# Performance work log

Measured on AMD Instinct MI355X. Metric: run time of the kernel, lower is better.

Reference implementation:

```python
import jax, jax.numpy as jnp
import numpy as np

RADIUS = 16.0
N_SLOT = 112
N_HEAD = 8
DIM = 512
EPS = 1e-5  # LayerNorm eps (torch default)


def _l2norm(x, axis):
    # F.normalize: x / max(||x||, 1e-12)
    n = jnp.linalg.norm(x, axis=axis, keepdims=True)
    return x / jnp.maximum(n, 1e-12)


def _layernorm(x, g, b):
    m = jnp.mean(x, axis=-1, keepdims=True)
    v = jnp.var(x, axis=-1, keepdims=True)
    return (x - m) * jax.lax.rsqrt(v + EPS) * g + b


def setup_inputs() -> dict:
    key = jax.random.key(0)
    ks = jax.random.split(key, 8)
    B, S = 64, 512
    head_dim = 512 // N_HEAD
    return {
        "query": jax.random.normal(ks[0], (B, S, DIM), jnp.float32),
        "value": jax.random.normal(ks[1], (B, S, 512), jnp.float32),
        # learned memory (init normal(0, 0.5) as in the module)
        "mem_key": jax.random.normal(ks[2], (N_HEAD * N_SLOT, head_dim), jnp.float32) * 0.5,
        "mem_value": jax.random.normal(ks[3], (N_SLOT, 512), jnp.float32) * 0.5,
        # linear projections (weight stored torch-style as [out, in])
        "q_w": jax.random.normal(ks[4], (512, DIM), jnp.float32) * 0.02,
        "q_b": jnp.zeros((512,), jnp.float32),
        "v_w": jax.random.normal(ks[5], (512, 512), jnp.float32) * 0.02,
        "v_b": jnp.zeros((512,), jnp.float32),
        "out_w": jax.random.normal(ks[6], (512, 512 * N_HEAD), jnp.float32) * 0.02,
        "out_b": jnp.zeros((512,), jnp.float32),
        "ln1_g": jnp.ones((512,), jnp.float32),
        "ln1_b": jnp.zeros((512,), jnp.float32),
        "ln3_g": jnp.ones((512,), jnp.float32),
        "ln3_b": jnp.zeros((512,), jnp.float32),
    }


def reference(query, value, mem_key, mem_value, q_w, q_b, v_w, v_b,
              out_w, out_b, ln1_g, ln1_b, ln3_g, ln3_b):
    B, S, C = query.shape
    N = B * S
    # --- predict branch: multi-head cosine-sim addressing + softmax read ---
    key_n = _l2norm(mem_key.reshape(N_HEAD, N_SLOT, -1), axis=2)          # [h,s,d]
    qp = (query.reshape(N, C) @ q_w.T + q_b).reshape(N, N_HEAD, -1)       # [n,h,d]
    qp = _l2norm(qp, axis=2)
    key_sim = jnp.einsum('bhd,hsd->bhs', qp, key_n)                       # [n,h,slot]
    key_addr = jax.nn.softmax(RADIUS * key_sim, axis=2)
    m_head = jnp.einsum('bhs,sd->bhd', key_addr,
                        jax.lax.stop_gradient(mem_value))                 # value.detach()
    m_head = m_head.reshape(N, N_HEAD * 512)
    attn_out = m_head @ out_w.T + out_b                                   # [n,512]
    # dropout treated as identity (eval mode)
    f_predict = _layernorm(query + attn_out.reshape(B, S, -1), ln1_g, ln1_b)
    # --- recon branch (inference=False) ---
    v_flat = jax.lax.stop_gradient(value.reshape(N, -1))                  # value.detach()
    v_proj = v_flat @ v_w.T + v_b
    value_norm = _l2norm(mem_value, axis=1)                               # [slot,512]
    value_sim = _l2norm(v_proj, axis=1) @ value_norm.T                    # [n,slot]
    value_addr = jax.nn.softmax(RADIUS * value_sim, axis=1)
    attn_recon = value_addr @ mem_value                                   # [n,512]
    contrastive_loss = jnp.abs(jnp.eye(N_SLOT, dtype=mem_value.dtype)
                               - value_norm @ value_norm.T).sum() * 0.01
    cos = jnp.sum(_l2norm(attn_recon, 1) * _l2norm(v_flat, 1), axis=1)
    recon_loss = jnp.abs(1.0 - cos).sum() / N
    attn_recon = _layernorm(attn_recon, ln3_g, ln3_b)
    f_target_recon = _layernorm(query + attn_recon.reshape(B, S, -1), ln1_g, ln1_b)
    return (f_predict, f_target_recon, recon_loss, contrastive_loss)
```

## Files before the change

### kernel.cpp

```cpp
#include <hip/hip_runtime.h>
#include <hip/hip_bf16.h>
#include <math.h>

typedef __bf16 bf16_t;
typedef __attribute__((ext_vector_type(8))) __bf16 bf16x8;
typedef __attribute__((ext_vector_type(4))) __bf16 bf16x4;
typedef __attribute__((ext_vector_type(4))) float f32x4;

#define LN_EPS 1e-5f
#define RADIUS_F 16.0f

__device__ inline bf16x8 zero8() {
    bf16x8 v;
#pragma unroll
    for (int i = 0; i < 8; ++i) v[i] = (__bf16)0.f;
    return v;
}

__device__ inline float wave_sum(float v) {
#pragma unroll
    for (int o = 1; o < 64; o <<= 1) v += __shfl_xor(v, o);
    return v;
}

__device__ inline void gload_lds16(const bf16_t* g, bf16_t* l) {
    __builtin_amdgcn_global_load_lds(
        (const __attribute__((address_space(1))) void*)g,
        (__attribute__((address_space(3))) void*)l, 16, 0, 0);
}

__device__ inline void drain_barrier() {
    asm volatile("s_waitcnt vmcnt(0)" ::: "memory");
    __builtin_amdgcn_s_barrier();
}

__global__ __launch_bounds__(256) void cast_all(
    const float* __restrict__ q, const float* __restrict__ v,
    const float* __restrict__ qw, const float* __restrict__ vw,
    const float* __restrict__ ow,
    bf16_t* __restrict__ qb, bf16_t* __restrict__ vb,
    bf16_t* __restrict__ qwb, bf16_t* __restrict__ vwb,
    bf16_t* __restrict__ owb) {
    const int total = 9043968;
    for (int i = blockIdx.x * 256 + threadIdx.x; i < total; i += gridDim.x * 256) {
        const float* src;
        bf16_t* dst;
        int j;
        if (i < 4194304) { src = q; dst = qb; j = i; }
        else if (i < 8388608) { src = v; dst = vb; j = i - 4194304; }
        else if (i < 8454144) { src = qw; dst = qwb; j = i - 8388608; }
        else if (i < 8519680) { src = vw; dst = vwb; j = i - 8454144; }
        else { src = ow; dst = owb; j = i - 8519680; }
        float4 x = reinterpret_cast<const float4*>(src)[j];
        bf16x4 o;
        o[0] = (__bf16)x.x; o[1] = (__bf16)x.y; o[2] = (__bf16)x.z; o[3] = (__bf16)x.w;
        reinterpret_cast<bf16x4*>(dst)[j] = o;
    }
}

__global__ __launch_bounds__(256) void keyn_k(const float* __restrict__ mk,
                                              bf16_t* __restrict__ kn) {
    int row = blockIdx.x * 4 + (threadIdx.x >> 6);
    int lane = threadIdx.x & 63;
    float x = mk[(size_t)row * 64 + lane];
    float ss = wave_sum(x * x);
    kn[(size_t)row * 64 + lane] = (__bf16)(x / fmaxf(sqrtf(ss), 1e-12f));
}

__global__ __launch_bounds__(256) void mv_prep_k(const float* __restrict__ mv,
                                                 bf16_t* __restrict__ mvb,
                                                 bf16_t* __restrict__ mvT,
                                                 float* __restrict__ invmv,
                                                 float* __restrict__ loss_slots) {
    const int s = blockIdx.x, tid = threadIdx.x;
    if (s >= 112) {
        mvb[(size_t)s * 512 + tid * 2] = (__bf16)0.f;
        mvb[(size_t)s * 512 + tid * 2 + 1] = (__bf16)0.f;
        mvT[(size_t)tid * 128 + s] = (__bf16)0.f;
        mvT[(size_t)(tid + 256) * 128 + s] = (__bf16)0.f;
        return;
    }
    float2 x = *reinterpret_cast<const float2*>(mv + (size_t)s * 512 + tid * 2);
    float ss = wave_sum(x.x * x.x + x.y * x.y);
    __shared__ float red[4];
    int wid = tid >> 6, lane = tid & 63;
    if (lane == 0) red[wid] = ss;
    __syncthreads();
    ss = red[0] + red[1] + red[2] + red[3];
    if (tid == 0) invmv[s] = 1.f / fmaxf(sqrtf(ss), 1e-12f);
    mvb[(size_t)s * 512 + tid * 2] = (__bf16)x.x;
    mvb[(size_t)s * 512 + tid * 2 + 1] = (__bf16)x.y;
    mvT[(size_t)tid * 128 + s] = (__bf16)mv[(size_t)s * 512 + tid];
    mvT[(size_t)(tid + 256) * 128 + s] = (__bf16)mv[(size_t)s * 512 + tid + 256];
    if (s == 0 && tid < 2) loss_slots[tid] = 0.f;
}

__global__ __launch_bounds__(256) void contrastive_k(const float* __restrict__ mv,
                                                     const float* __restrict__ invmv,
                                                     float* __restrict__ out_slot) {
    const int a = blockIdx.x;
    const int tid = threadIdx.x, wid = tid >> 6, lane = tid & 63;
    __shared__ float rowa[512];
    __shared__ float wsum[4];
    for (int i = tid; i < 512; i += 256) rowa[i] = mv[(size_t)a * 512 + i];
    __syncthreads();
    float acc = 0.f;
    const float ia = invmv[a];
    for (int b = wid; b < 112; b += 4) {
        float d = 0.f;
#pragma unroll
        for (int i = 0; i < 8; ++i) d += rowa[lane + i * 64] * mv[(size_t)b * 512 + lane + i * 64];
        d = wave_sum(d);
        float gv = d * ia * invmv[b];
        acc += fabsf((a == b ? 1.f : 0.f) - gv);
    }
    if (lane == 0) wsum[wid] = acc;
    __syncthreads();
    if (tid == 0) atomicAdd(out_slot, (wsum[0] + wsum[1] + wsum[2] + wsum[3]) * 0.01f);
}

__global__ __launch_bounds__(256) void gemm128_bb(
    const bf16_t* __restrict__ A, int lda,
    const bf16_t* __restrict__ W, int ldw,
    const float* __restrict__ bias,
    bf16_t* __restrict__ Cb, int ldc, int K) {
    __shared__ __align__(16) bf16_t As[2][128 * 32];
    __shared__ __align__(16) bf16_t Bs[2][128 * 32];
    const int tid = threadIdx.x;
    const int wid = tid >> 6, lane = tid & 63;
    const int wr = wid >> 1, wc = wid & 1;
    const int lr = lane & 15;
    const int ko = (lane >> 4) * 8;
    const size_t rowBase = (size_t)blockIdx.x * 128;
    const size_t colBase = (size_t)blockIdx.y * 128;
    const int r0 = tid >> 2;
    const int c0 = (tid & 3) * 8;
    const bf16_t* a_src = A + (rowBase + r0) * lda + c0;
    const bf16_t* w_src = W + (colBase + r0) * ldw + c0;
    f32x4 acc[4][4];
#pragma unroll
    for (int m = 0; m < 4; ++m)
#pragma unroll
        for (int n = 0; n < 4; ++n) {
            acc[m][n][0] = 0.f; acc[m][n][1] = 0.f;
            acc[m][n][2] = 0.f; acc[m][n][3] = 0.f;
        }
    auto stage = [&](int buf, int ks) {
        const int k0 = ks * 32;
        gload_lds16(a_src + k0, &As[buf][tid * 8]);
        gload_lds16(a_src + (size_t)64 * lda + k0, &As[buf][2048 + tid * 8]);
        gload_lds16(w_src + k0, &Bs[buf][tid * 8]);
        gload_lds16(w_src + (size_t)64 * ldw + k0, &Bs[buf][2048 + tid * 8]);
    };
    stage(0, 0);
    __syncthreads();
    const int nt = K >> 5;
    int cur = 0;
    for (int ks = 0; ks < nt; ++ks) {
        const int nb = cur ^ 1;
        if (ks + 1 < nt) stage(nb, ks + 1);
        bf16x8 af[4], bfr[4];
#pragma unroll
        for (int m = 0; m < 4; ++m)
            af[m] = *reinterpret_cast<const bf16x8*>(&As[cur][(wr * 64 + m * 16 + lr) * 32 + ko]);
#pragma unroll
        for (int n = 0; n < 4; ++n)
            bfr[n] = *reinterpret_cast<const bf16x8*>(&Bs[cur][(wc * 64 + n * 16 + lr) * 32 + ko]);
#pragma unroll
        for (int m = 0; m < 4; ++m)
#pragma unroll
            for (int n = 0; n < 4; ++n)
                acc[m][n] = __builtin_amdgcn_mfma_f32_16x16x32_bf16(af[m], bfr[n], acc[m][n], 0, 0, 0);
        __syncthreads();
        cur = nb;
    }
    const int rj = (lane >> 4) * 4;
#pragma unroll
    for (int n = 0; n < 4; ++n) {
        const int col = (int)colBase + wc * 64 + n * 16 + lr;
        const float bv = bias ? bias[col] : 0.f;
#pragma unroll
        for (int m = 0; m < 4; ++m) {
            const size_t r = rowBase + wr * 64 + m * 16 + rj;
#pragma unroll
            for (int j = 0; j < 4; ++j)
                Cb[(r + j) * ldc + col] = (__bf16)(acc[m][n][j] + bv);
        }
    }
}

__global__ __launch_bounds__(256) void gemm_bt(
    const bf16_t* __restrict__ A, int lda, int aZ,
    const bf16_t* __restrict__ W, int ldw, int wZ,
    bf16_t* __restrict__ Cb, int ldc, int cZ,
    int M, int N, int K) {
    const int wid = threadIdx.x >> 6;
    const int lane = threadIdx.x & 63;
    const int lr = lane & 15;
    const int kk = (lane >> 4) * 8;
    const int row0 = blockIdx.x * 64 + wid * 16;
    const int col0 = blockIdx.y * 64;
    A += (size_t)blockIdx.z * aZ;
    W += (size_t)blockIdx.z * wZ;
    const bf16_t* a_ptr = A + (size_t)(row0 + lr) * lda + kk;
    const bf16_t* w_ptr = W + (size_t)(col0 + lr) * ldw + kk;
    f32x4 acc[4];
#pragma unroll
    for (int t = 0; t < 4; ++t) { acc[t][0] = 0.f; acc[t][1] = 0.f; acc[t][2] = 0.f; acc[t][3] = 0.f; }
    bool colv[4];
#pragma unroll
    for (int t = 0; t < 4; ++t) colv[t] = (col0 + t * 16 + lr) < N;
    for (int k0 = 0; k0 < K; k0 += 32) {
        bf16x8 a = *reinterpret_cast<const bf16x8*>(a_ptr + k0);
#pragma unroll
        for (int t = 0; t < 4; ++t) {
            bf16x8 b;
            if (colv[t]) b = *reinterpret_cast<const bf16x8*>(w_ptr + (size_t)t * 16 * ldw + k0);
            else b = zero8();
            acc[t] = __builtin_amdgcn_mfma_f32_16x16x32_bf16(a, b, acc[t], 0, 0, 0);
        }
    }
    const int rb = (lane >> 4) * 4;
    Cb += (size_t)blockIdx.z * cZ;
#pragma unroll
    for (int t = 0; t < 4; ++t) {
        int col = col0 + t * 16 + lr;
        if (col >= N) continue;
#pragma unroll
        for (int j = 0; j < 4; ++j) {
            int r = row0 + rb + j;
            Cb[(size_t)r * ldc + col] = (__bf16)acc[t][j];
        }
    }
}

__global__ __launch_bounds__(256) void addr_predict(const bf16_t* __restrict__ qp,
                                                    const bf16_t* __restrict__ keyn,
                                                    bf16_t* __restrict__ addr) {
    const int wid = threadIdx.x >> 6, lane = threadIdx.x & 63;
    const int lr = lane & 15, kk = (lane >> 4) * 8;
    const int h = blockIdx.y;
    const int row0 = blockIdx.x * 64 + wid * 16;
    const bf16_t* a_ptr = qp + (size_t)(row0 + lr) * 512 + h * 64 + kk;
    bf16x8 a0 = *reinterpret_cast<const bf16x8*>(a_ptr);
    bf16x8 a1 = *reinterpret_cast<const bf16x8*>(a_ptr + 32);
    float ssq = 0.f;
#pragma unroll
    for (int j = 0; j < 8; ++j) {
        float x = (float)a0[j], y = (float)a1[j];
        ssq += x * x + y * y;
    }
    ssq += __shfl_xor(ssq, 16);
    ssq += __shfl_xor(ssq, 32);
    const float invq = 1.f / fmaxf(sqrtf(ssq), 1e-12f);
    f32x4 acc[7];
#pragma unroll
    for (int t = 0; t < 7; ++t) {
        const bf16_t* b_ptr = keyn + (size_t)(h * 112 + t * 16 + lr) * 64 + kk;
        bf16x8 b0 = *reinterpret_cast<const bf16x8*>(b_ptr);
        bf16x8 b1 = *reinterpret_cast<const bf16x8*>(b_ptr + 32);
        f32x4 c; c[0] = 0.f; c[1] = 0.f; c[2] = 0.f; c[3] = 0.f;
        c = __builtin_amdgcn_mfma_f32_16x16x32_bf16(a0, b0, c, 0, 0, 0);
        c = __builtin_amdgcn_mfma_f32_16x16x32_bf16(a1, b1, c, 0, 0, 0);
        acc[t] = c;
    }
    const int rb = (lane >> 4) * 4;
    float iq[4];
#pragma unroll
    for (int j = 0; j < 4; ++j) iq[j] = __shfl(invq, rb + j);
#pragma unroll
    for (int j = 0; j < 4; ++j) {
        float m = -1e30f;
#pragma unroll
        for (int t = 0; t < 7; ++t) { acc[t][j] *= iq[j] * RADIUS_F; m = fmaxf(m, acc[t][j]); }
#pragma unroll
        for (int o = 1; o < 16; o <<= 1) m = fmaxf(m, __shfl_xor(m, o));
        float s = 0.f;
#pragma unroll
        for (int t = 0; t < 7; ++t) { float e = __expf(acc[t][j] - m); acc[t][j] = e; s += e; }
#pragma unroll
        for (int o = 1; o < 16; o <<= 1) s += __shfl_xor(s, o);
        const float rs = 1.f / s;
#pragma unroll
        for (int t = 0; t < 7; ++t) acc[t][j] *= rs;
    }
#pragma unroll
    for (int t = 0; t < 7; ++t)
#pragma unroll
        for (int j = 0; j < 4; ++j)
            addr[(size_t)(row0 + rb + j) * 896 + h * 112 + t * 16 + lr] = (__bf16)acc[t][j];
}

__global__ __launch_bounds__(256, 2) void gemm_sim_softmax(
    const bf16_t* __restrict__ vp,
    const bf16_t* __restrict__ mvb,
    const float* __restrict__ invmv,
    bf16_t* __restrict__ addr2) {
    __shared__ __align__(16) bf16_t As[2][128 * 32];
    __shared__ __align__(16) bf16_t Bs[2][128 * 32];
    const int tid = threadIdx.x;
    const int wid = tid >> 6, lane = tid & 63;
    const int lr = lane & 15, hi = lane >> 4;
    const int ko = hi * 8;
    const size_t rowBase = (size_t)blockIdx.x * 128;
    const int r0 = tid >> 2, c0 = (tid & 3) * 8;
    const bf16_t* a_src = vp + (rowBase + r0) * 512 + c0;
    const bf16_t* b_src = mvb + (size_t)r0 * 512 + c0;
    f32x4 acc[2][8];
#pragma unroll
    for (int m = 0; m < 2; ++m)
#pragma unroll
        for (int n = 0; n < 8; ++n) {
            acc[m][n][0] = 0.f; acc[m][n][1] = 0.f;
            acc[m][n][2] = 0.f; acc[m][n][3] = 0.f;
        }
    float ssq[2] = {0.f, 0.f};
    auto stage = [&](int buf, int ks) {
        const int k0 = ks * 32;
        gload_lds16(a_src + k0, &As[buf][tid * 8]);
        gload_lds16(a_src + (size_t)64 * 512 + k0, &As[buf][2048 + tid * 8]);
        gload_lds16(b_src + k0, &Bs[buf][tid * 8]);
        gload_lds16(b_src + (size_t)64 * 512 + k0, &Bs[buf][2048 + tid * 8]);
    };
    stage(0, 0);
    drain_barrier();
    int cur = 0;
    for (int ks = 0; ks < 16; ++ks) {
        if (ks < 15) stage(cur ^ 1, ks + 1);
        bf16x8 af[2], bfr[8];
#pragma unroll
        for (int m = 0; m < 2; ++m)
            af[m] = *reinterpret_cast<const bf16x8*>(&As[cur][(wid * 32 + m * 16 + lr) * 32 + ko]);
#pragma unroll
        for (int n = 0; n < 8; ++n)
            bfr[n] = *reinterpret_cast<const bf16x8*>(&Bs[cur][(n * 16 + lr) * 32 + ko]);
#pragma unroll
        for (int m = 0; m < 2; ++m) {
#pragma unroll
            for (int j = 0; j < 8; ++j) { float x = (float)af[m][j]; ssq[m] += x * x; }
#pragma unroll
            for (int n = 0; n < 8; ++n)
                acc[m][n] = __builtin_amdgcn_mfma_f32_16x16x32_bf16(af[m], bfr[n], acc[m][n], 0, 0, 0);
        }
        drain_barrier();
        cur ^= 1;
    }
#pragma unroll
    for (int m = 0; m < 2; ++m) {
        ssq[m] += __shfl_xor(ssq[m], 16);
        ssq[m] += __shfl_xor(ssq[m], 32);
        ssq[m] = 1.f / fmaxf(sqrtf(ssq[m]), 1e-12f);
    }
    const int rb = hi * 4;
    float imv[7];
#pragma unroll
    for (int n = 0; n < 7; ++n) imv[n] = invmv[n * 16 + lr];
#pragma unroll
    for (int m = 0; m < 2; ++m)
#pragma unroll
        for (int j = 0; j < 4; ++j) {
            const float iq = __shfl(ssq[m], (lane & 48) | (rb + j));
            float x[7];
            float mx = -1e30f;
#pragma unroll
            for (int n = 0; n < 7; ++n) {
                x[n] = acc[m][n][j] * iq * imv[n] * RADIUS_F;
                mx = fmaxf(mx, x[n]);
            }
#pragma unroll
            for (int o = 1; o < 16; o <<= 1) mx = fmaxf(mx, __shfl_xor(mx, o));
            float s = 0.f;
#pragma unroll
            for (int n = 0; n < 7; ++n) { x[n] = __expf(x[n] - mx); s += x[n]; }
#pragma unroll
            for (int o = 1; o < 16; o <<= 1) s += __shfl_xor(s, o);
            const float rs = 1.f / s;
            const size_t row = rowBase + wid * 32 + m * 16 + rb + j;
#pragma unroll
            for (int n = 0; n < 7; ++n)
                addr2[row * 128 + n * 16 + lr] = (__bf16)(x[n] * rs);
            addr2[row * 128 + 112 + lr] = (__bf16)0.f;
        }
}

__global__ __launch_bounds__(256) void fused_ep(
    const bf16_t* __restrict__ sP, const bf16_t* __restrict__ sR,
    const bf16_t* __restrict__ qb, const bf16_t* __restrict__ vb,
    const float* __restrict__ g1, const float* __restrict__ b1,
    const float* __restrict__ g3, const float* __restrict__ b3,
    float* __restrict__ fP, float* __restrict__ fR,
    float* __restrict__ rrpart) {
    const int wid = threadIdx.x >> 6, lane = threadIdx.x & 63;
    const size_t row0 = (size_t)blockIdx.x * 8 + wid * 2;
    const int c1 = lane * 8, c2 = lane * 8 + 4;
    float xP[2][8], aR[2][8], qv[2][8];
    float s1[2], s2[2], sa[2], sa2[2], sav[2], sv2[2];
#pragma unroll
    for (int r = 0; r < 2; ++r) {
        const size_t base = (row0 + r) * 512;
        bf16x8 p = *reinterpret_cast<const bf16x8*>(sP + base + c1);
        bf16x8 rr = *reinterpret_cast<const bf16x8*>(sR + base + c1);
        bf16x8 qq = *reinterpret_cast<const bf16x8*>(qb + base + c1);
        bf16x8 vv = *reinterpret_cast<const bf16x8*>(vb + base + c1);
        s1[r] = 0.f; s2[r] = 0.f;
        sa[r] = 0.f; sa2[r] = 0.f; sav[r] = 0.f; sv2[r] = 0.f;
#pragma unroll
        for (int j = 0; j < 8; ++j) {
            const float qf = (float)qq[j];
            const float pf = (float)p[j];
            const float af = (float)rr[j];
            const float vf = (float)vv[j];
            qv[r][j] = qf;
            const float x = qf + pf;
            xP[r][j] = x;
            s1[r] += x; s2[r] += x * x;
            aR[r][j] = af;
            sa[r] += af; sa2[r] += af * af;
            sav[r] += af * vf; sv2[r] += vf * vf;
        }
    }
#pragma unroll
    for (int o = 1; o < 64; o <<= 1)
#pragma unroll
        for (int r = 0; r < 2; ++r) {
            s1[r] += __shfl_xor(s1[r], o);
            s2[r] += __shfl_xor(s2[r], o);
            sa[r] += __shfl_xor(sa[r], o);
            sa2[r] += __shfl_xor(sa2[r], o);
            sav[r] += __shfl_xor(sav[r], o);
            sv2[r] += __shfl_xor(sv2[r], o);
        }
    const float4 g1a = *reinterpret_cast<const float4*>(g1 + c1);
    const float4 g1b = *reinterpret_cast<const float4*>(g1 + c2);
    const float4 b1a = *reinterpret_cast<const float4*>(b1 + c1);
    const float4 b1b = *reinterpret_cast<const float4*>(b1 + c2);
#pragma unroll
    for (int r = 0; r < 2; ++r) {
        const size_t base = (row0 + r) * 512;
        const float mu = s1[r] * (1.f / 512.f);
        const float rs = rsqrtf(s2[r] * (1.f / 512.f) - mu * mu + LN_EPS);
        float4 o1 = make_float4((xP[r][0] - mu) * rs * g1a.x + b1a.x,
                                (xP[r][1] - mu) * rs * g1a.y + b1a.y,
                                (xP[r][2] - mu) * rs * g1a.z + b1a.z,
                                (xP[r][3] - mu) * rs * g1a.w + b1a.w);
        float4 o2 = make_float4((xP[r][4] - mu) * rs * g1b.x + b1b.x,
                                (xP[r][5] - mu) * rs * g1b.y + b1b.y,
                                (xP[r][6] - mu) * rs * g1b.z + b1b.z,
                                (xP[r][7] - mu) * rs * g1b.w + b1b.w);
        *reinterpret_cast<float4*>(fP + base + c1) = o1;
        *reinterpret_cast<float4*>(fP + base + c2) = o2;
    }
    float rrw = 0.f;
    if (lane == 0) {
#pragma unroll
        for (int r = 0; r < 2; ++r) {
            const float na = fmaxf(sqrtf(sa2[r]), 1e-12f);
            const float nv = fmaxf(sqrtf(sv2[r]), 1e-12f);
            rrw += fabsf(1.f - sav[r] / (na * nv));
        }
    }
    const float4 g3a = *reinterpret_cast<const float4*>(g3 + c1);
    const float4 g3b = *reinterpret_cast<const float4*>(g3 + c2);
    const float4 b3a = *reinterpret_cast<const float4*>(b3 + c1);
    const float4 b3b = *reinterpret_cast<const float4*>(b3 + c2);
#pragma unroll
    for (int r = 0; r < 2; ++r) {
        const float mu3 = sa[r] * (1.f / 512.f);
        const float r3 = rsqrtf(sa2[r] * (1.f / 512.f) - mu3 * mu3 + LN_EPS);
        float s1n = 0.f, s2n = 0.f;
        const float gg[8] = {g3a.x, g3a.y, g3a.z, g3a.w, g3b.x, g3b.y, g3b.z, g3b.w};
        const float bb[8] = {b3a.x, b3a.y, b3a.z, b3a.w, b3b.x, b3b.y, b3b.z, b3b.w};
#pragma unroll
        for (int j = 0; j < 8; ++j) {
            const float x = qv[r][j] + (aR[r][j] - mu3) * r3 * gg[j] + bb[j];
            aR[r][j] = x;
            s1n += x; s2n += x * x;
        }
        s1[r] = s1n; s2[r] = s2n;
    }
#pragma unroll
    for (int o = 1; o < 64; o <<= 1)
#pragma unroll
        for (int r = 0; r < 2; ++r) {
            s1[r] += __shfl_xor(s1[r], o);
            s2[r] += __shfl_xor(s2[r], o);
        }
#pragma unroll
    for (int r = 0; r < 2; ++r) {
        const size_t base = (row0 + r) * 512;
        const float mu = s1[r] * (1.f / 512.f);
        const float rs = rsqrtf(s2[r] * (1.f / 512.f) - mu * mu + LN_EPS);
        float4 o1 = make_float4((aR[r][0] - mu) * rs * g1a.x + b1a.x,
                                (aR[r][1] - mu) * rs * g1a.y + b1a.y,
                                (aR[r][2] - mu) * rs * g1a.z + b1a.z,
                                (aR[r][3] - mu) * rs * g1a.w + b1a.w);
        float4 o2 = make_float4((aR[r][4] - mu) * rs * g1b.x + b1b.x,
                                (aR[r][5] - mu) * rs * g1b.y + b1b.y,
                                (aR[r][6] - mu) * rs * g1b.z + b1b.z,
                                (aR[r][7] - mu) * rs * g1b.w + b1b.w);
        *reinterpret_cast<float4*>(fR + base + c1) = o1;
        *reinterpret_cast<float4*>(fR + base + c2) = o2;
    }
    __shared__ float rred[4];
    if (lane == 0) rred[wid] = rrw;
    __syncthreads();
    if (threadIdx.x == 0)
        rrpart[blockIdx.x] = rred[0] + rred[1] + rred[2] + rred[3];
}

__global__ __launch_bounds__(256) void reduce_part_k(const float* __restrict__ part,
                                                     int n, float* __restrict__ out) {
    float s = 0.f;
    for (int i = threadIdx.x; i < n; i += 256) s += part[i];
    s = wave_sum(s);
    __shared__ float red[4];
    const int wid = threadIdx.x >> 6, lane = threadIdx.x & 63;
    if (lane == 0) red[wid] = s;
    __syncthreads();
    if (threadIdx.x == 0)
        out[0] = (red[0] + red[1] + red[2] + red[3]) * (1.f / 32768.f);
}

extern "C" void kernel_launch(void* const* d_in, const int* in_sizes, int n_in,
                              void* d_out, int out_size, void* d_ws, size_t ws_size,
                              hipStream_t stream) {
    const float* query = (const float*)d_in[0];
    const float* value = (const float*)d_in[1];
    const float* mem_key = (const float*)d_in[2];
    const float* mem_value = (const float*)d_in[3];
    const float* q_w = (const float*)d_in[4];
    const float* q_b = (const float*)d_in[5];
    const float* v_w = (const float*)d_in[6];
    const float* v_b = (const float*)d_in[7];
    const float* out_w = (const float*)d_in[8];
    const float* out_b = (const float*)d_in[9];
    const float* ln1_g = (const float*)d_in[10];
    const float* ln1_b = (const float*)d_in[11];
    const float* ln3_g = (const float*)d_in[12];
    const float* ln3_b = (const float*)d_in[13];
    float* out = (float*)d_out;

    char* ws = (char*)d_ws;
    size_t off = 0;
    auto alloc = [&](size_t bytes) {
        void* p = ws + off;
        off += (bytes + 255) & ~(size_t)255;
        return p;
    };
    bf16_t* qb = (bf16_t*)alloc(16777216ull * 2);
    bf16_t* vb = (bf16_t*)alloc(16777216ull * 2);
    bf16_t* qpb = (bf16_t*)alloc(16777216ull * 2);
    bf16_t* vpb = (bf16_t*)alloc(16777216ull * 2);
    bf16_t* addr = (bf16_t*)alloc(32768ull * 896 * 2);
    bf16_t* qwb = (bf16_t*)alloc(262144ull * 2);
    bf16_t* vwb = (bf16_t*)alloc(262144ull * 2);
    bf16_t* owb = (bf16_t*)alloc(2097152ull * 2);
    bf16_t* wct = (bf16_t*)alloc(896ull * 512 * 2);
    bf16_t* keyn = (bf16_t*)alloc(896ull * 64 * 2);
    bf16_t* mvb = (bf16_t*)alloc(128ull * 512 * 2);
    bf16_t* mvT = (bf16_t*)alloc(512ull * 128 * 2);
    float* invmv = (float*)alloc(112 * 4);
    float* rrpart = (float*)alloc(4096 * 4);
    bf16_t* addr2 = addr;
    bf16_t* stageP = qpb;
    bf16_t* stageR = vpb;

    float* f_predict = out;
    float* f_recon = out + 16777216;
    float* loss_slots = out + 33554432;

    cast_all<<<2048, 256, 0, stream>>>(query, value, q_w, v_w, out_w,
                                       qb, vb, qwb, vwb, owb);
    keyn_k<<<224, 256, 0, stream>>>(mem_key, keyn);
    mv_prep_k<<<128, 256, 0, stream>>>(mem_value, mvb, mvT, invmv, loss_slots);
    contrastive_k<<<112, 256, 0, stream>>>(mem_value, invmv, loss_slots + 1);
    gemm_bt<<<dim3(8, 2, 8), 256, 0, stream>>>(owb, 4096, 512, mvb, 512, 0,
                                               wct, 896, 112, 512, 112, 512);
    gemm128_bb<<<dim3(256, 4), 256, 0, stream>>>(qb, 512, qwb, 512, q_b,
                                                 qpb, 512, 512);
    gemm128_bb<<<dim3(256, 4), 256, 0, stream>>>(vb, 512, vwb, 512, v_b,
                                                 vpb, 512, 512);
    addr_predict<<<dim3(512, 8), 256, 0, stream>>>(qpb, keyn, addr);
    gemm128_bb<<<dim3(256, 4), 256, 0, stream>>>(addr, 896, wct, 896, out_b,
                                                 stageP, 512, 896);
    gemm_sim_softmax<<<256, 256, 0, stream>>>(vpb, mvb, invmv, addr2);
    gemm128_bb<<<dim3(256, 4), 256, 0, stream>>>(addr2, 128, mvT, 128,
                                                 (const float*)nullptr,
                                                 stageR, 512, 128);
    fused_ep<<<4096, 256, 0, stream>>>(stageP, stageR, qb, vb,
                                       ln1_g, ln1_b, ln3_g, ln3_b,
                                       f_predict, f_recon, rrpart);
    reduce_part_k<<<1, 256, 0, stream>>>(rrpart, 4096, loss_slots);
}
```

Baseline: 325.0 us.

## Batch paired GEMMs into dual-problem launches and halve sim-softmax row tile

Merges the query/value projection GEMMs into one launch indexed by blockIdx.z, and likewise the predict output GEMM with the recon readout GEMM. This needs a separate addr2 buffer so the two no longer alias. The sim-softmax kernel now covers 64 rows per block instead of 128, doubling its grid to 512 blocks, and its occupancy hint is dropped. The goal is fewer launches and better GPU fill when small GEMMs run side by side. The cost is one more workspace buffer and a grid that mixes blocks with K=896 and K=128, which may balance poorly.

```diff
diff --git a/kernel.cpp b/kernel.cpp
--- a/kernel.cpp
+++ b/kernel.cpp
@@ -119,11 +119,18 @@
     if (tid == 0) atomicAdd(out_slot, (wsum[0] + wsum[1] + wsum[2] + wsum[3]) * 0.01f);
 }
 
-__global__ __launch_bounds__(256) void gemm128_bb(
-    const bf16_t* __restrict__ A, int lda,
-    const bf16_t* __restrict__ W, int ldw,
-    const float* __restrict__ bias,
-    bf16_t* __restrict__ Cb, int ldc, int K) {
+__global__ __launch_bounds__(256) void gemm_dual(
+    const bf16_t* __restrict__ A0, int lda0, const bf16_t* __restrict__ W0, int ldw0,
+    const float* __restrict__ bias0, bf16_t* __restrict__ C0, int K0,
+    const bf16_t* __restrict__ A1, int lda1, const bf16_t* __restrict__ W1, int ldw1,
+    const float* __restrict__ bias1, bf16_t* __restrict__ C1, int K1) {
+    const bf16_t* A = blockIdx.z ? A1 : A0;
+    const bf16_t* W = blockIdx.z ? W1 : W0;
+    const float* bias = blockIdx.z ? bias1 : bias0;
+    bf16_t* Cb = blockIdx.z ? C1 : C0;
+    const int lda = blockIdx.z ? lda1 : lda0;
+    const int ldw = blockIdx.z ? ldw1 : ldw0;
+    const int K = blockIdx.z ? K1 : K0;
     __shared__ __align__(16) bf16_t As[2][128 * 32];
     __shared__ __align__(16) bf16_t Bs[2][128 * 32];
     const int tid = threadIdx.x;
@@ -184,7 +191,7 @@
             const size_t r = rowBase + wr * 64 + m * 16 + rj;
 #pragma unroll
             for (int j = 0; j < 4; ++j)
-                Cb[(r + j) * ldc + col] = (__bf16)(acc[m][n][j] + bv);
+                Cb[(r + j) * 512 + col] = (__bf16)(acc[m][n][j] + bv);
         }
     }
 }
@@ -291,34 +298,30 @@
             addr[(size_t)(row0 + rb + j) * 896 + h * 112 + t * 16 + lr] = (__bf16)acc[t][j];
 }
 
-__global__ __launch_bounds__(256, 2) void gemm_sim_softmax(
+__global__ __launch_bounds__(256) void gemm_sim_softmax(
     const bf16_t* __restrict__ vp,
     const bf16_t* __restrict__ mvb,
     const float* __restrict__ invmv,
     bf16_t* __restrict__ addr2) {
-    __shared__ __align__(16) bf16_t As[2][128 * 32];
+    __shared__ __align__(16) bf16_t As[2][64 * 32];
     __shared__ __align__(16) bf16_t Bs[2][128 * 32];
     const int tid = threadIdx.x;
     const int wid = tid >> 6, lane = tid & 63;
     const int lr = lane & 15, hi = lane >> 4;
     const int ko = hi * 8;
-    const size_t rowBase = (size_t)blockIdx.x * 128;
+    const size_t rowBase = (size_t)blockIdx.x * 64;
     const int r0 = tid >> 2, c0 = (tid & 3) * 8;
     const bf16_t* a_src = vp + (rowBase + r0) * 512 + c0;
     const bf16_t* b_src = mvb + (size_t)r0 * 512 + c0;
-    f32x4 acc[2][8];
-#pragma unroll
-    for (int m = 0; m < 2; ++m)
-#pragma unroll
-        for (int n = 0; n < 8; ++n) {
-            acc[m][n][0] = 0.f; acc[m][n][1] = 0.f;
-            acc[m][n][2] = 0.f; acc[m][n][3] = 0.f;
-        }
-    float ssq[2] = {0.f, 0.f};
+    f32x4 acc[8];
+#pragma unroll
+    for (int n = 0; n < 8; ++n) {
+        acc[n][0] = 0.f; acc[n][1] = 0.f; acc[n][2] = 0.f; acc[n][3] = 0.f;
+    }
+    float ssq = 0.f;
     auto stage = [&](int buf, int ks) {
         const int k0 = ks * 32;
         gload_lds16(a_src + k0, &As[buf][tid * 8]);
-        gload_lds16(a_src + (size_t)64 * 512 + k0, &As[buf][2048 + tid * 8]);
         gload_lds16(b_src + k0, &Bs[buf][tid * 8]);
         gload_lds16(b_src + (size_t)64 * 512 + k0, &Bs[buf][2048 + tid * 8]);
     };
@@ -327,60 +330,50 @@
     int cur = 0;
     for (int ks = 0; ks < 16; ++ks) {
         if (ks < 15) stage(cur ^ 1, ks + 1);
-        bf16x8 af[2], bfr[8];
-#pragma unroll
-        for (int m = 0; m < 2; ++m)
-            af[m] = *reinterpret_cast<const bf16x8*>(&As[cur][(wid * 32 + m * 16 + lr) * 32 + ko]);
+        bf16x8 af, bfr[8];
+        af = *reinterpret_cast<const bf16x8*>(&As[cur][(wid * 16 + lr) * 32 + ko]);
 #pragma unroll
         for (int n = 0; n < 8; ++n)
             bfr[n] = *reinterpret_cast<const bf16x8*>(&Bs[cur][(n * 16 + lr) * 32 + ko]);
 #pragma unroll
-        for (int m = 0; m < 2; ++m) {
-#pragma unroll
-            for (int j = 0; j < 8; ++j) { float x = (float)af[m][j]; ssq[m] += x * x; }
-#pragma unroll
-            for (int n = 0; n < 8; ++n)
-                acc[m][n] = __builtin_amdgcn_mfma_f32_16x16x32_bf16(af[m], bfr[n], acc[m][n], 0, 0, 0);
-        }
+        for (int j = 0; j < 8; ++j) { float x = (float)af[j]; ssq += x * x; }
+#pragma unroll
+        for (int n = 0; n < 8; ++n)
+            acc[n] = __builtin_amdgcn_mfma_f32_16x16x32_bf16(af, bfr[n], acc[n], 0, 0, 0);
         drain_barrier();
         cur ^= 1;
     }
-#pragma unroll
-    for (int m = 0; m < 2; ++m) {
-        ssq[m] += __shfl_xor(ssq[m], 16);
-        ssq[m] += __shfl_xor(ssq[m], 32);
-        ssq[m] = 1.f / fmaxf(sqrtf(ssq[m]), 1e-12f);
-    }
+    ssq += __shfl_xor(ssq, 16);
+    ssq += __shfl_xor(ssq, 32);
+    ssq = 1.f / fmaxf(sqrtf(ssq), 1e-12f);
     const int rb = hi * 4;
     float imv[7];
 #pragma unroll
     for (int n = 0; n < 7; ++n) imv[n] = invmv[n * 16 + lr];
 #pragma unroll
-    for (int m = 0; m < 2; ++m)
-#pragma unroll
-        for (int j = 0; j < 4; ++j) {
-            const float iq = __shfl(ssq[m], (lane & 48) | (rb + j));
-            float x[7];
-            float mx = -1e30f;
-#pragma unroll
-            for (int n = 0; n < 7; ++n) {
-                x[n] = acc[m][n][j] * iq * imv[n] * RADIUS_F;
-                mx = fmaxf(mx, x[n]);
-            }
-#pragma unroll
-            for (int o = 1; o < 16; o <<= 1) mx = fmaxf(mx, __shfl_xor(mx, o));
-            float s = 0.f;
-#pragma unroll
-            for (int n = 0; n < 7; ++n) { x[n] = __expf(x[n] - mx); s += x[n]; }
-#pragma unroll
-            for (int o = 1; o < 16; o <<= 1) s += __shfl_xor(s, o);
-            const float rs = 1.f / s;
-            const size_t row = rowBase + wid * 32 + m * 16 + rb + j;
-#pragma unroll
-            for (int n = 0; n < 7; ++n)
-                addr2[row * 128 + n * 16 + lr] = (__bf16)(x[n] * rs);
-            addr2[row * 128 + 112 + lr] = (__bf16)0.f;
-        }
+    for (int j = 0; j < 4; ++j) {
+        const float iq = __shfl(ssq, (lane & 48) | (rb + j));
+        float x[7];
+        float mx = -1e30f;
+#pragma unroll
+        for (int n = 0; n < 7; ++n) {
+            x[n] = acc[n][j] * iq * imv[n] * RADIUS_F;
+            mx = fmaxf(mx, x[n]);
+        }
+#pragma unroll
+        for (int o = 1; o < 16; o <<= 1) mx = fmaxf(mx, __shfl_xor(mx, o));
+        float s = 0.f;
+#pragma unroll
+        for (int n = 0; n < 7; ++n) { x[n] = __expf(x[n] - mx); s += x[n]; }
+#pragma unroll
+        for (int o = 1; o < 16; o <<= 1) s += __shfl_xor(s, o);
+        const float rs = 1.f / s;
+        const size_t row = rowBase + wid * 16 + rb + j;
+#pragma unroll
+        for (int n = 0; n < 7; ++n)
+            addr2[row * 128 + n * 16 + lr] = (__bf16)(x[n] * rs);
+        addr2[row * 128 + 112 + lr] = (__bf16)0.f;
+    }
 }
 
 __global__ __launch_bounds__(256) void fused_ep(
@@ -552,6 +545,7 @@
     bf16_t* qpb = (bf16_t*)alloc(16777216ull * 2);
     bf16_t* vpb = (bf16_t*)alloc(16777216ull * 2);
     bf16_t* addr = (bf16_t*)alloc(32768ull * 896 * 2);
+    bf16_t* addr2 = (bf16_t*)alloc(32768ull * 128 * 2);
     bf16_t* qwb = (bf16_t*)alloc(262144ull * 2);
     bf16_t* vwb = (bf16_t*)alloc(262144ull * 2);
     bf16_t* owb = (bf16_t*)alloc(2097152ull * 2);
@@ -561,7 +555,6 @@
     bf16_t* mvT = (bf16_t*)alloc(512ull * 128 * 2);
     float* invmv = (float*)alloc(112 * 4);
     float* rrpart = (float*)alloc(4096 * 4);
-    bf16_t* addr2 = addr;
     bf16_t* stageP = qpb;
     bf16_t* stageR = vpb;
 
@@ -576,17 +569,14 @@
     contrastive_k<<<112, 256, 0, stream>>>(mem_value, invmv, loss_slots + 1);
     gemm_bt<<<dim3(8, 2, 8), 256, 0, stream>>>(owb, 4096, 512, mvb, 512, 0,
                                                wct, 896, 112, 512, 112, 512);
-    gemm128_bb<<<dim3(256, 4), 256, 0, stream>>>(qb, 512, qwb, 512, q_b,
-                                                 qpb, 512, 512);
-    gemm128_bb<<<dim3(256, 4), 256, 0, stream>>>(vb, 512, vwb, 512, v_b,
-                                                 vpb, 512, 512);
+    gemm_dual<<<dim3(256, 4, 2), 256, 0, stream>>>(
+        qb, 512, qwb, 512, q_b, qpb, 512,
+        vb, 512, vwb, 512, v_b, vpb, 512);
     addr_predict<<<dim3(512, 8), 256, 0, stream>>>(qpb, keyn, addr);
-    gemm128_bb<<<dim3(256, 4), 256, 0, stream>>>(addr, 896, wct, 896, out_b,
-                                                 stageP, 512, 896);
-    gemm_sim_softmax<<<256, 256, 0, stream>>>(vpb, mvb, invmv, addr2);
-    gemm128_bb<<<dim3(256, 4), 256, 0, stream>>>(addr2, 128, mvT, 128,
-                                                 (const float*)nullptr,
-                                                 stageR, 512, 128);
+    gemm_sim_softmax<<<512, 256, 0, stream>>>(vpb, mvb, invmv, addr2);
+    gemm_dual<<<dim3(256, 4, 2), 256, 0, stream>>>(
+        addr, 896, wct, 896, out_b, stageP, 896,
+        addr2, 128, mvT, 128, (const float*)nullptr, stageR, 128);
     fused_ep<<<4096, 256, 0, stream>>>(stageP, stageR, qb, vb,
                                        ln1_g, ln1_b, ln3_g, ln3_b,
                                        f_predict, f_recon, rrpart);
```

After: 307.8 us. 5.3% less time.
